# Kernel tuning notes

Measured on AMD Instinct MI355X. Metric: run time of the kernel, lower is better.

## Reference

```python
import jax, jax.numpy as jnp
import numpy as np

N = 100_000
E = 16 * N  # avg degree 16
B = 64


def _linear_params(key, fan_in, fan_out, mode='kaiming'):
    # kaiming_uniform_ (nonlinearity='relu'): bound = sqrt(6/fan_in)
    # xavier_uniform_: bound = sqrt(6/(fan_in+fan_out))
    if mode == 'kaiming':
        bound = np.sqrt(6.0 / fan_in)
    else:
        bound = np.sqrt(6.0 / (fan_in + fan_out))
    w = jax.random.uniform(key, (fan_in, fan_out), jnp.float32, -bound, bound)
    b = jnp.zeros((fan_out,), jnp.float32)
    return w, b


def setup_inputs() -> dict:
    key = jax.random.key(0)
    ks = jax.random.split(key, 12)
    pos = jax.random.normal(ks[0], (N, 3), jnp.float32) * 10.0
    # edges: every node is a destination (deg=16 each), random sources
    src = jax.random.randint(ks[1], (E,), 0, N, jnp.int32)
    dst = jnp.repeat(jnp.arange(N, dtype=jnp.int32), E // N)
    edge_index = jnp.stack([src, dst], axis=0)  # [2, E], row0=j(src), row1=i(dst)
    batch = jnp.sort(jax.random.randint(ks[2], (N,), 0, B, jnp.int32))
    timestep = jax.random.normal(ks[3], (B,), jnp.float32)
    w1a, b1a = _linear_params(ks[4], 3 + 3, 64)
    w1b, b1b = _linear_params(ks[5], 64, 64)
    w2a, b2a = _linear_params(ks[6], 64 + 3, 64)
    w2b, b2b = _linear_params(ks[7], 64, 64)
    w3a, b3a = _linear_params(ks[8], 64 + 3, 128)
    w3b, b3b = _linear_params(ks[9], 128, 128)
    wr1, br1 = _linear_params(ks[10], 128, 64, mode='xavier')
    wr2, br2 = _linear_params(ks[11], 64, 1, mode='xavier')
    return {
        'pos': pos, 'edge_index': edge_index, 'batch': batch, 'timestep': timestep,
        'w1a': w1a, 'b1a': b1a, 'w1b': w1b, 'b1b': b1b,
        'w2a': w2a, 'b2a': b2a, 'w2b': w2b, 'b2b': b2b,
        'w3a': w3a, 'b3a': b3a, 'w3b': w3b, 'b3b': b3b,
        'wr1': wr1, 'br1': br1, 'wr2': wr2, 'br2': br2,
    }


def _pointnet_layer(h, pos, src, dst, wa, ba, wb, bb):
    # message: MLP(concat(h_j, pos_j - pos_i)); aggregate: max over incoming edges
    edge_feat = jnp.concatenate([h[src], pos[src] - pos[dst]], axis=-1)  # [E, C+3]
    msg = jnp.maximum(edge_feat @ wa + ba, 0.0) @ wb + bb               # [E, C_out]
    agg = jax.ops.segment_max(msg, dst, num_segments=N)                  # [N, C_out]
    return jnp.where(jnp.isfinite(agg), agg, 0.0)  # nodes w/o edges -> 0


def reference(pos, edge_index, batch, timestep,
              w1a, b1a, w1b, b1b, w2a, b2a, w2b, b2b,
              w3a, b3a, w3b, b3b, wr1, br1, wr2, br2):
    src, dst = edge_index[0], edge_index[1]
    h = jax.nn.relu(_pointnet_layer(pos, pos, src, dst, w1a, b1a, w1b, b1b))
    h = jax.nn.relu(_pointnet_layer(h, pos, src, dst, w2a, b2a, w2b, b2b))
    h = jax.nn.relu(_pointnet_layer(h, pos, src, dst, w3a, b3a, w3b, b3b))
    # global mean pool
    sums = jax.ops.segment_sum(h, batch, num_segments=B)          # [B, 128]
    counts = jax.ops.segment_sum(jnp.ones((h.shape[0],), h.dtype), batch, num_segments=B)
    pooled = sums / jnp.maximum(counts, 1.0)[:, None]
    out = (pooled @ wr1 + br1) @ wr2 + br2                        # [B, 1]
    return jax.nn.sigmoid(out).squeeze(-1)                        # [B]
```

## Files before the change

### kernel.cpp

```cpp
#include <hip/hip_runtime.h>
#include <math.h>

#define NNODES 100000
#define NEDGES 1600000
#define NBATCH 64
#define NTILES (NEDGES/64)

typedef __attribute__((ext_vector_type(8))) short  short8;
typedef __attribute__((ext_vector_type(4))) short  short4v;
typedef __attribute__((ext_vector_type(2))) unsigned int uint2v;
typedef __attribute__((ext_vector_type(4))) float  float4v;
typedef unsigned short ushort_t;

__device__ __forceinline__ short f2bf(float f) {
    unsigned u = __builtin_bit_cast(unsigned, f);
    u += 0x7fffu + ((u >> 16) & 1u);
    return (short)(u >> 16);
}
__device__ __forceinline__ float b2f(short s) {
    unsigned u = ((unsigned)(unsigned short)s) << 16;
    return __builtin_bit_cast(float, u);
}
__device__ __forceinline__ unsigned cvt_pk_bf16(float lo, float hi) {
    unsigned r;
    asm("v_cvt_pk_bf16_f32 %0, %1, %2" : "=v"(r) : "v"(lo), "v"(hi));
    return r;
}
__device__ __forceinline__ float red_groups_max(float m) {
    unsigned a = __builtin_bit_cast(unsigned, m), b = a;
    asm("v_permlane16_swap_b32 %0, %1" : "+v"(a), "+v"(b));
    m = fmaxf(__builtin_bit_cast(float, a), __builtin_bit_cast(float, b));
    a = __builtin_bit_cast(unsigned, m); b = a;
    asm("v_permlane32_swap_b32 %0, %1" : "+v"(a), "+v"(b));
    return fmaxf(__builtin_bit_cast(float, a), __builtin_bit_cast(float, b));
}

__device__ __forceinline__ void barrier_lds_only() {
    asm volatile("s_waitcnt lgkmcnt(0)" ::: "memory");
    __builtin_amdgcn_sched_barrier(0);
    __builtin_amdgcn_s_barrier();
    __builtin_amdgcn_sched_barrier(0);
}

template<int CIN, int H, int O, int NWAVES, int MINW>
__global__ __launch_bounds__(NWAVES*64, MINW)
void layer_mfma(const ushort_t* __restrict__ hin, const float* __restrict__ pos,
                const int* __restrict__ srcArr,
                const float* __restrict__ wa, const float* __restrict__ ba,
                const float* __restrict__ wb, const float* __restrict__ bb,
                ushort_t* __restrict__ hout)
{
    constexpr int K1   = CIN + 3;
    constexpr int S1   = ((K1 + 31) / 32) * 32;
    constexpr int NS1  = S1 / 32;
    constexpr int NS2  = H / 32;
    constexpr int HB1  = H / 32;
    constexpr int EH1  = NWAVES / HB1;
    constexpr int E1   = 64 / EH1;
    constexpr int NT1  = E1 / 16;
    constexpr int CB2  = O / 32;
    constexpr int EH2  = NWAVES / CB2;
    constexpr int E2   = 64 / EH2;
    constexpr int MT2  = E2 / 16;
    constexpr int RSX  = S1 + 8;
    constexpr int RSY  = H + 8;

    __shared__ short smem[64 * RSX + 64 * RSY];
    short* xs = smem;
    short* ys = smem + 64 * RSX;

    const int tid  = threadIdx.x;
    const int lane = tid & 63;
    const int w    = tid >> 6;
    const int g    = lane >> 4;
    const int c    = lane & 15;
    const int e    = tid & 63;
    const int rep  = tid >> 6;
    const int hb   = w / EH1;
    const int eg1  = w % EH1;
    const int cb2  = w / EH2;
    const int eg2  = w % EH2;
    const int STRIDE = gridDim.x;

    {
        short4v z4 = (short4v)0;
        for (int i = tid; i < (64*RSX + 64*RSY)/4; i += NWAVES*64)
            ((short4v*)smem)[i] = z4;
    }

    int srcN = srcArr[blockIdx.x * 64 + e];
    short8 pA;
    float ps0, ps1, ps2, pd0, pd1, pd2;
    auto issue = [&](int targ) {
        const int src = srcN;
        if constexpr (CIN == 3) {
            if (rep == 0) {
                ps0 = pos[src*3+0]; ps1 = pos[src*3+1]; ps2 = pos[src*3+2];
                const int node = targ*4 + (e >> 4);
                pd0 = pos[node*3+0]; pd1 = pos[node*3+1]; pd2 = pos[node*3+2];
            }
        } else {
            pA = *(const short8*)(hin + (size_t)src * CIN + rep*8);
            if (rep == 0) {
                ps0 = pos[src*3+0]; ps1 = pos[src*3+1]; ps2 = pos[src*3+2];
                const int node = targ*4 + (e >> 4);
                pd0 = pos[node*3+0]; pd1 = pos[node*3+1]; pd2 = pos[node*3+2];
            }
        }
        const int tn = min(targ + STRIDE, NTILES - 1);
        srcN = srcArr[tn*64 + e];
    };
    issue(blockIdx.x);

    short8 wah[2][NS1];
    float  bav[2][4];
    #pragma unroll
    for (int mt = 0; mt < 2; ++mt) {
        const int h = hb*32 + mt*16 + c;
        #pragma unroll
        for (int pk = 0; pk < NS1; ++pk) {
            short8 fh;
            #pragma unroll
            for (int j = 0; j < 8; ++j) {
                const int k = pk*32 + g*8 + j;
                fh[j] = (k < K1) ? f2bf(wa[k*H + h]) : (short)0;
            }
            wah[mt][pk] = fh;
        }
        #pragma unroll
        for (int r = 0; r < 4; ++r) bav[mt][r] = ba[hb*32 + mt*16 + g*4 + r];
    }
    short8 wbh[2][NS2];
    float  bbsc[2];
    #pragma unroll
    for (int cb = 0; cb < 2; ++cb) {
        const int o = cb2*32 + cb*16 + c;
        #pragma unroll
        for (int pk = 0; pk < NS2; ++pk) {
            short8 fh;
            #pragma unroll
            for (int j = 0; j < 8; ++j) {
                const int k = pk*32 + g*8 + j;
                fh[j] = f2bf(wb[k*O + o]);
            }
            wbh[cb][pk] = fh;
        }
        bbsc[cb] = bb[o];
    }
    __syncthreads();

    for (int tile = blockIdx.x; tile < NTILES; tile += STRIDE) {
        if constexpr (CIN == 3) {
            if (rep == 0) {
                short8 hv;
                hv[0] = f2bf(ps0); hv[1] = f2bf(ps1); hv[2] = f2bf(ps2);
                hv[3] = f2bf(ps0 - pd0);
                hv[4] = f2bf(ps1 - pd1);
                hv[5] = f2bf(ps2 - pd2);
                hv[6] = 0; hv[7] = 0;
                *(short8*)(xs + e*RSX) = hv;
            }
        } else {
            *(short8*)(xs + e*RSX + rep*8) = pA;
            if (rep == 0) {
                short8 hv;
                hv[0] = f2bf(ps0 - pd0);
                hv[1] = f2bf(ps1 - pd1);
                hv[2] = f2bf(ps2 - pd2);
                hv[3]=0; hv[4]=0; hv[5]=0; hv[6]=0; hv[7]=0;
                *(short8*)(xs + e*RSX + CIN) = hv;
            }
        }
        barrier_lds_only();

        issue(min(tile + STRIDE, NTILES - 1));

        {
            float4v C1[2][NT1];
            #pragma unroll
            for (int mt = 0; mt < 2; ++mt)
                #pragma unroll
                for (int nt = 0; nt < NT1; ++nt)
                    #pragma unroll
                    for (int r = 0; r < 4; ++r) C1[mt][nt][r] = bav[mt][r];
            #pragma unroll
            for (int pk = 0; pk < NS1; ++pk)
                #pragma unroll
                for (int nt = 0; nt < NT1; ++nt) {
                    short8 xh = *(const short8*)(xs + (eg1*E1 + nt*16 + c)*RSX + pk*32 + g*8);
                    #pragma unroll
                    for (int mt = 0; mt < 2; ++mt)
                        C1[mt][nt] = __builtin_amdgcn_mfma_f32_16x16x32_bf16(wah[mt][pk], xh, C1[mt][nt], 0,0,0);
                }
            #pragma unroll
            for (int mt = 0; mt < 2; ++mt)
                #pragma unroll
                for (int nt = 0; nt < NT1; ++nt) {
                    uint2v pv;
                    pv[0] = cvt_pk_bf16(fmaxf(C1[mt][nt][0], 0.f), fmaxf(C1[mt][nt][1], 0.f));
                    pv[1] = cvt_pk_bf16(fmaxf(C1[mt][nt][2], 0.f), fmaxf(C1[mt][nt][3], 0.f));
                    *(uint2v*)(ys + (eg1*E1 + nt*16 + c)*RSY + hb*32 + mt*16 + g*4) = pv;
                }
        }
        barrier_lds_only();

        float4v C2[MT2][2];
        #pragma unroll
        for (int mt = 0; mt < MT2; ++mt)
            #pragma unroll
            for (int cb = 0; cb < 2; ++cb)
                #pragma unroll
                for (int r = 0; r < 4; ++r) C2[mt][cb][r] = bbsc[cb];
        #pragma unroll
        for (int pk = 0; pk < NS2; ++pk)
            #pragma unroll
            for (int mt = 0; mt < MT2; ++mt) {
                short8 yh = *(const short8*)(ys + (eg2*E2 + mt*16 + c)*RSY + pk*32 + g*8);
                #pragma unroll
                for (int cb = 0; cb < 2; ++cb)
                    C2[mt][cb] = __builtin_amdgcn_mfma_f32_16x16x32_bf16(yh, wbh[cb][pk], C2[mt][cb], 0,0,0);
            }
        #pragma unroll
        for (int mt = 0; mt < MT2; ++mt)
            #pragma unroll
            for (int cb = 0; cb < 2; ++cb) {
                float m = fmaxf(fmaxf(C2[mt][cb][0], C2[mt][cb][1]),
                                fmaxf(C2[mt][cb][2], C2[mt][cb][3]));
                m = red_groups_max(m);
                if (lane < 16) {
                    const int node = tile*4 + eg2*(E2/16) + mt;
                    hout[(size_t)node*O + cb2*32 + cb*16 + lane] = (ushort_t)f2bf(fmaxf(m, 0.f));
                }
            }
    }
}

__global__ void zero_k(float* __restrict__ p, int n)
{
    const int i = blockIdx.x * 256 + threadIdx.x;
    if (i < n) p[i] = 0.f;
}

__global__ void pool_k(const ushort_t* __restrict__ h3, const int* __restrict__ batch,
                       float* __restrict__ pooled, float* __restrict__ counts)
{
    const int c    = threadIdx.x & 127;
    const int half = threadIdx.x >> 7;
    const int nbeg = blockIdx.x * 128 + half * 64;
    if (nbeg >= NNODES) return;
    const int nend = min(nbeg + 64, NNODES);

    int   cur = batch[nbeg];
    float acc = 0.f;
    int   runlen = 0;
    for (int n = nbeg; n < nend; ++n) {
        const int b = batch[n];
        if (b != cur) {
            atomicAdd(pooled + cur*128 + c, acc);
            if (c == 0) atomicAdd(counts + cur, (float)runlen);
            acc = 0.f; runlen = 0; cur = b;
        }
        acc += b2f((short)h3[(size_t)n * 128 + c]);
        ++runlen;
    }
    atomicAdd(pooled + cur*128 + c, acc);
    if (c == 0) atomicAdd(counts + cur, (float)runlen);
}

__global__ void reg_k(const float* __restrict__ pooled, const float* __restrict__ counts,
                      const float* __restrict__ wr1, const float* __restrict__ br1,
                      const float* __restrict__ wr2, const float* __restrict__ br2,
                      float* __restrict__ out)
{
    const int b = blockIdx.x;
    const int h = threadIdx.x;
    const float rc = 1.f / fmaxf(counts[b], 1.f);
    float acc = br1[h];
    #pragma unroll
    for (int k = 0; k < 128; ++k)
        acc = fmaf(pooled[b*128 + k] * rc, wr1[k*64 + h], acc);
    float v = acc * wr2[h];
    #pragma unroll
    for (int s = 1; s < 64; s <<= 1)
        v += __shfl_xor(v, s);
    if (h == 0) out[b] = 1.f / (1.f + expf(-(v + br2[0])));
}

extern "C" void kernel_launch(void* const* d_in, const int* in_sizes, int n_in,
                              void* d_out, int out_size, void* d_ws, size_t ws_size,
                              hipStream_t stream)
{
    const float* pos   = (const float*)d_in[0];
    const int*   eidx  = (const int*)d_in[1];
    const int*   batch = (const int*)d_in[2];
    const float *w1a = (const float*)d_in[4],  *b1a = (const float*)d_in[5];
    const float *w1b = (const float*)d_in[6],  *b1b = (const float*)d_in[7];
    const float *w2a = (const float*)d_in[8],  *b2a = (const float*)d_in[9];
    const float *w2b = (const float*)d_in[10], *b2b = (const float*)d_in[11];
    const float *w3a = (const float*)d_in[12], *b3a = (const float*)d_in[13];
    const float *w3b = (const float*)d_in[14], *b3b = (const float*)d_in[15];
    const float *wr1 = (const float*)d_in[16], *br1 = (const float*)d_in[17];
    const float *wr2 = (const float*)d_in[18], *br2 = (const float*)d_in[19];
    const int* srcArr = eidx;

    ushort_t* h1 = (ushort_t*)d_ws;
    ushort_t* h2 = h1 + (size_t)NNODES * 64;
    ushort_t* h3 = h2 + (size_t)NNODES * 64;
    float* pooled = (float*)(h3 + (size_t)NNODES * 128);
    float* counts = pooled + NBATCH * 128;
    float* out    = (float*)d_out;

    layer_mfma<3,  64, 64, 4, 6><<<1536, dim3(256), 0, stream>>>(nullptr, pos, srcArr, w1a, b1a, w1b, b1b, h1);
    layer_mfma<64, 64, 64, 8, 4><<< 512, dim3(512), 0, stream>>>(h1,      pos, srcArr, w2a, b2a, w2b, b2b, h2);
    layer_mfma<64, 128,128,8, 4><<< 512, dim3(512), 0, stream>>>(h2,      pos, srcArr, w3a, b3a, w3b, b3b, h3);
    zero_k<<<(NBATCH*128 + NBATCH + 255)/256, dim3(256), 0, stream>>>(pooled, NBATCH*128 + NBATCH);
    pool_k<<<(NNODES + 127)/128, dim3(256), 0, stream>>>(h3, batch, pooled, counts);
    reg_k <<<NBATCH, dim3(64), 0, stream>>>(pooled, counts, wr1, br1, wr2, br2, out);
}
```

Baseline: 357.4 us.

## Double-buffer LDS and software-pipeline the two GEMM stages across tiles

The per-tile loop is restructured so the second GEMM and max-reduction of the previous tile run in the same phase as the first GEMM of the current tile. The staged inputs for the next tile are written into alternate LDS buffers. This cuts the LDS barriers per tile from two to one and lets MFMA work from both stages interleave. In exchange, LDS use doubles and there is a prologue/epilogue. The first layer's launch drops from 1536 to 1024 blocks and its template parameter goes from 6 to 4, likely to match the lower occupancy the larger LDS footprint allows.

```diff
diff --git a/kernel.cpp b/kernel.cpp
--- a/kernel.cpp
+++ b/kernel.cpp
@@ -64,10 +64,10 @@
     constexpr int MT2  = E2 / 16;
     constexpr int RSX  = S1 + 8;
     constexpr int RSY  = H + 8;
-
-    __shared__ short smem[64 * RSX + 64 * RSY];
-    short* xs = smem;
-    short* ys = smem + 64 * RSX;
+    constexpr int XSZ  = 64 * RSX;
+    constexpr int YSZ  = 64 * RSY;
+
+    __shared__ short smem[2*(XSZ + YSZ)];
 
     const int tid  = threadIdx.x;
     const int lane = tid & 63;
@@ -84,7 +84,7 @@
 
     {
         short4v z4 = (short4v)0;
-        for (int i = tid; i < (64*RSX + 64*RSY)/4; i += NWAVES*64)
+        for (int i = tid; i < (2*(XSZ + YSZ))/4; i += NWAVES*64)
             ((short4v*)smem)[i] = z4;
     }
 
@@ -149,7 +149,7 @@
     }
     __syncthreads();
 
-    for (int tile = blockIdx.x; tile < NTILES; tile += STRIDE) {
+    auto stage = [&](short* xsd) {
         if constexpr (CIN == 3) {
             if (rep == 0) {
                 short8 hv;
@@ -158,52 +158,50 @@
                 hv[4] = f2bf(ps1 - pd1);
                 hv[5] = f2bf(ps2 - pd2);
                 hv[6] = 0; hv[7] = 0;
-                *(short8*)(xs + e*RSX) = hv;
+                *(short8*)(xsd + e*RSX) = hv;
             }
         } else {
-            *(short8*)(xs + e*RSX + rep*8) = pA;
+            *(short8*)(xsd + e*RSX + rep*8) = pA;
             if (rep == 0) {
                 short8 hv;
                 hv[0] = f2bf(ps0 - pd0);
                 hv[1] = f2bf(ps1 - pd1);
                 hv[2] = f2bf(ps2 - pd2);
                 hv[3]=0; hv[4]=0; hv[5]=0; hv[6]=0; hv[7]=0;
-                *(short8*)(xs + e*RSX + CIN) = hv;
-            }
-        }
-        barrier_lds_only();
-
-        issue(min(tile + STRIDE, NTILES - 1));
-
-        {
-            float4v C1[2][NT1];
-            #pragma unroll
-            for (int mt = 0; mt < 2; ++mt)
+                *(short8*)(xsd + e*RSX + CIN) = hv;
+            }
+        }
+    };
+
+    auto g1 = [&](const short* xsr, short* ysw) {
+        float4v C1[2][NT1];
+        #pragma unroll
+        for (int mt = 0; mt < 2; ++mt)
+            #pragma unroll
+            for (int nt = 0; nt < NT1; ++nt)
                 #pragma unroll
-                for (int nt = 0; nt < NT1; ++nt)
-                    #pragma unroll
-                    for (int r = 0; r < 4; ++r) C1[mt][nt][r] = bav[mt][r];
-            #pragma unroll
-            for (int pk = 0; pk < NS1; ++pk)
+                for (int r = 0; r < 4; ++r) C1[mt][nt][r] = bav[mt][r];
+        #pragma unroll
+        for (int pk = 0; pk < NS1; ++pk)
+            #pragma unroll
+            for (int nt = 0; nt < NT1; ++nt) {
+                short8 xh = *(const short8*)(xsr + (eg1*E1 + nt*16 + c)*RSX + pk*32 + g*8);
                 #pragma unroll
-                for (int nt = 0; nt < NT1; ++nt) {
-                    short8 xh = *(const short8*)(xs + (eg1*E1 + nt*16 + c)*RSX + pk*32 + g*8);
-                    #pragma unroll
-                    for (int mt = 0; mt < 2; ++mt)
-                        C1[mt][nt] = __builtin_amdgcn_mfma_f32_16x16x32_bf16(wah[mt][pk], xh, C1[mt][nt], 0,0,0);
-                }
-            #pragma unroll
-            for (int mt = 0; mt < 2; ++mt)
-                #pragma unroll
-                for (int nt = 0; nt < NT1; ++nt) {
-                    uint2v pv;
-                    pv[0] = cvt_pk_bf16(fmaxf(C1[mt][nt][0], 0.f), fmaxf(C1[mt][nt][1], 0.f));
-                    pv[1] = cvt_pk_bf16(fmaxf(C1[mt][nt][2], 0.f), fmaxf(C1[mt][nt][3], 0.f));
-                    *(uint2v*)(ys + (eg1*E1 + nt*16 + c)*RSY + hb*32 + mt*16 + g*4) = pv;
-                }
-        }
-        barrier_lds_only();
-
+                for (int mt = 0; mt < 2; ++mt)
+                    C1[mt][nt] = __builtin_amdgcn_mfma_f32_16x16x32_bf16(wah[mt][pk], xh, C1[mt][nt], 0,0,0);
+            }
+        #pragma unroll
+        for (int mt = 0; mt < 2; ++mt)
+            #pragma unroll
+            for (int nt = 0; nt < NT1; ++nt) {
+                uint2v pv;
+                pv[0] = cvt_pk_bf16(fmaxf(C1[mt][nt][0], 0.f), fmaxf(C1[mt][nt][1], 0.f));
+                pv[1] = cvt_pk_bf16(fmaxf(C1[mt][nt][2], 0.f), fmaxf(C1[mt][nt][3], 0.f));
+                *(uint2v*)(ysw + (eg1*E1 + nt*16 + c)*RSY + hb*32 + mt*16 + g*4) = pv;
+            }
+    };
+
+    auto g2 = [&](const short* ysr, int outTile) {
         float4v C2[MT2][2];
         #pragma unroll
         for (int mt = 0; mt < MT2; ++mt)
@@ -215,7 +213,7 @@
         for (int pk = 0; pk < NS2; ++pk)
             #pragma unroll
             for (int mt = 0; mt < MT2; ++mt) {
-                short8 yh = *(const short8*)(ys + (eg2*E2 + mt*16 + c)*RSY + pk*32 + g*8);
+                short8 yh = *(const short8*)(ysr + (eg2*E2 + mt*16 + c)*RSY + pk*32 + g*8);
                 #pragma unroll
                 for (int cb = 0; cb < 2; ++cb)
                     C2[mt][cb] = __builtin_amdgcn_mfma_f32_16x16x32_bf16(yh, wbh[cb][pk], C2[mt][cb], 0,0,0);
@@ -228,10 +226,35 @@
                                 fmaxf(C2[mt][cb][2], C2[mt][cb][3]));
                 m = red_groups_max(m);
                 if (lane < 16) {
-                    const int node = tile*4 + eg2*(E2/16) + mt;
+                    const int node = outTile*4 + eg2*(E2/16) + mt;
                     hout[(size_t)node*O + cb2*32 + cb*16 + lane] = (ushort_t)f2bf(fmaxf(m, 0.f));
                 }
             }
+    };
+
+    stage(smem);
+    issue(min(blockIdx.x + STRIDE, NTILES - 1));
+    barrier_lds_only();
+
+    int i = 0;
+    int prevTile = -1;
+    for (int tile = blockIdx.x; tile < NTILES; tile += STRIDE, ++i) {
+        const int q = i & 1;
+        short* xs_cur = smem + q*XSZ;
+        short* xs_nxt = smem + (q^1)*XSZ;
+        short* ys_cur = smem + 2*XSZ + q*YSZ;
+        short* ys_prv = smem + 2*XSZ + (q^1)*YSZ;
+
+        if (prevTile >= 0) g2(ys_prv, prevTile);
+        g1(xs_cur, ys_cur);
+        stage(xs_nxt);
+        issue(min(tile + 2*STRIDE, NTILES - 1));
+        barrier_lds_only();
+        prevTile = tile;
+    }
+    if (prevTile >= 0) {
+        const int qf = (i - 1) & 1;
+        g2(smem + 2*XSZ + qf*YSZ, prevTile);
     }
 }
 
@@ -310,7 +333,7 @@
     float* counts = pooled + NBATCH * 128;
     float* out    = (float*)d_out;
 
-    layer_mfma<3,  64, 64, 4, 6><<<1536, dim3(256), 0, stream>>>(nullptr, pos, srcArr, w1a, b1a, w1b, b1b, h1);
+    layer_mfma<3,  64, 64, 4, 4><<<1024, dim3(256), 0, stream>>>(nullptr, pos, srcArr, w1a, b1a, w1b, b1b, h1);
     layer_mfma<64, 64, 64, 8, 4><<< 512, dim3(512), 0, stream>>>(h1,      pos, srcArr, w2a, b2a, w2b, b2b, h2);
     layer_mfma<64, 128,128,8, 4><<< 512, dim3(512), 0, stream>>>(h2,      pos, srcArr, w3a, b3a, w3b, b3b, h3);
     zero_k<<<(NBATCH*128 + NBATCH + 255)/256, dim3(256), 0, stream>>>(pooled, NBATCH*128 + NBATCH);
```

New measurement: 329.8 us. 7.7% less time.
